# Optimization experiments

Measured on AMD Instinct MI355X. Metric: run time of the kernel, lower is better.

Reference implementation:

```python
import jax, jax.numpy as jnp
import numpy as np

EMB = 1024
HEADS = 16


def setup_inputs() -> dict:
    key = jax.random.key(0)
    ks = jax.random.split(key, 5)
    s = 1.0 / np.sqrt(EMB).astype(np.float32)
    return {
        "x": jax.random.normal(ks[0], (4, 2048, EMB), dtype=jnp.float32),
        "Wq": jax.random.normal(ks[1], (EMB, EMB), dtype=jnp.float32) * s,
        "bq": jnp.zeros((EMB,), dtype=jnp.float32),
        "Wk": jax.random.normal(ks[2], (EMB, EMB), dtype=jnp.float32) * s,
        "bk": jnp.zeros((EMB,), dtype=jnp.float32),
        "Wv": jax.random.normal(ks[3], (EMB, EMB), dtype=jnp.float32) * s,
        "bv": jnp.zeros((EMB,), dtype=jnp.float32),
        "Wo": jax.random.normal(ks[4], (EMB, EMB), dtype=jnp.float32) * s,
        "bo": jnp.zeros((EMB,), dtype=jnp.float32),
    }


def reference(x, Wq, bq, Wk, bk, Wv, bv, Wo, bo):
    b, n, e = x.shape
    h = HEADS
    d = e // h
    # QKV projections, split heads: [b, n, e] -> [b, h, n, d]
    def split_heads(t):
        return t.reshape(b, n, h, d).transpose(0, 2, 1, 3)
    q = split_heads(x @ Wq + bq)
    k = split_heads(x @ Wk + bk)
    v = split_heads(x @ Wv + bv)
    # NOTE: original scales by sqrt(emb_size), not sqrt(head_dim)
    energy = jnp.einsum('bhqd,bhkd->bhqk', q, k)
    att = jax.nn.softmax(energy / jnp.sqrt(jnp.float32(e)), axis=-1)
    # dropout is identity in eval mode
    out = jnp.einsum('bhqk,bhkd->bhqd', att, v)
    out = out.transpose(0, 2, 1, 3).reshape(b, n, e)
    return out @ Wo + bo
```

## Files before the change

### kernel.cpp

```cpp
#include <hip/hip_runtime.h>

#define EMB   1024
#define SEQ   2048
#define BATCH 4
#define HEADS 16
#define HDIM  64
#define MTOT  8192

typedef __bf16 bf16x8 __attribute__((ext_vector_type(8)));
typedef float  fx4    __attribute__((ext_vector_type(4)));

#if __has_builtin(__builtin_amdgcn_exp2f)
#define EXP2(x) __builtin_amdgcn_exp2f(x)
#else
#define EXP2(x) exp2f(x)
#endif

__device__ __forceinline__ unsigned short f2bf(float f) {
    unsigned u = __builtin_bit_cast(unsigned, f);
    u += 0x7fffu + ((u >> 16) & 1u);
    return (unsigned short)(u >> 16);
}
__device__ __forceinline__ unsigned short bfbits(float f) {
    __bf16 h = (__bf16)f;
    return __builtin_bit_cast(unsigned short, h);
}

#define AS1 __attribute__((address_space(1)))
#define AS3 __attribute__((address_space(3)))
__device__ __forceinline__ void glds16(const void* g, void* l) {
    __builtin_amdgcn_global_load_lds((AS1 void*)g, (AS3 void*)l, 16, 0, 0);
}
#define DRAIN_GLDS() __builtin_amdgcn_s_waitcnt(0x0f70)

#define BAR()    asm volatile("s_barrier" ::: "memory")
#define WAITV8() asm volatile("s_waitcnt vmcnt(8)" ::: "memory")
#define WAITV4() asm volatile("s_waitcnt vmcnt(4)" ::: "memory")
#define WAITV0() asm volatile("s_waitcnt vmcnt(0)" ::: "memory")

#define QSCALE 0.0450842137604569f

__global__ __launch_bounds__(256) void cvt_x_kernel(const float* __restrict__ x,
                                                    unsigned short* __restrict__ xb)
{
    const int idx = (blockIdx.x * 256 + threadIdx.x) * 4;
    const float4 v = *(const float4*)(x + idx);
    ushort4 o;
    o.x = f2bf(v.x); o.y = f2bf(v.y); o.z = f2bf(v.z); o.w = f2bf(v.w);
    *(ushort4*)(xb + idx) = o;
}

__global__ __launch_bounds__(256) void cvt_w_kernel(
    const float* __restrict__ w0, const float* __restrict__ w1,
    const float* __restrict__ w2, const float* __restrict__ w3,
    unsigned short* __restrict__ o0, unsigned short* __restrict__ o1,
    unsigned short* __restrict__ o2, unsigned short* __restrict__ o3)
{
    const int z = blockIdx.z;
    const float* W = z == 0 ? w0 : (z == 1 ? w1 : (z == 2 ? w2 : w3));
    unsigned short* O = z == 0 ? o0 : (z == 1 ? o1 : (z == 2 ? o2 : o3));

    __shared__ float Ws[64][65];
    const int t  = threadIdx.x;
    const int k0 = blockIdx.x * 64, n0 = blockIdx.y * 64;
#pragma unroll
    for (int p = 0; p < 4; ++p) {
        const int row = p * 16 + (t >> 4);
        const int col = (t & 15) * 4;
        const float4 v = *(const float4*)(W + (size_t)(k0 + row) * EMB + n0 + col);
        Ws[row][col]     = v.x; Ws[row][col + 1] = v.y;
        Ws[row][col + 2] = v.z; Ws[row][col + 3] = v.w;
    }
    __syncthreads();
    const int nn = t >> 2;
    const int kb = (t & 3) * 16;
#pragma unroll
    for (int q = 0; q < 2; ++q) {
        const int kk = kb + q * 8;
        ushort4 u0, u1;
        u0.x = f2bf(Ws[kk + 0][nn]); u0.y = f2bf(Ws[kk + 1][nn]);
        u0.z = f2bf(Ws[kk + 2][nn]); u0.w = f2bf(Ws[kk + 3][nn]);
        u1.x = f2bf(Ws[kk + 4][nn]); u1.y = f2bf(Ws[kk + 5][nn]);
        u1.z = f2bf(Ws[kk + 6][nn]); u1.w = f2bf(Ws[kk + 7][nn]);
        *(ushort4*)(O + (size_t)(n0 + nn) * EMB + k0 + kk)     = u0;
        *(ushort4*)(O + (size_t)(n0 + nn) * EMB + k0 + kk + 4) = u1;
    }
}

__global__ __launch_bounds__(512, 2) void gemm_qkv8p_kernel(
    const unsigned short* __restrict__ Xg, const unsigned short* __restrict__ Wg,
    const float* __restrict__ bq, const float* __restrict__ bk,
    const float* __restrict__ bv,
    unsigned short* __restrict__ qb, unsigned short* __restrict__ kb,
    unsigned short* __restrict__ vtb)
{
    __shared__ unsigned short Ls[4][2][128][64];

    int lin = blockIdx.x;
    lin = (lin & 7) * 48 + (lin >> 3);
    const int bx  = lin & 31;
    const int by  = lin >> 5;
    const int m0  = bx * 256;
    const int e0g = by * 256;

    const int t    = threadIdx.x;
    const int w    = t >> 6;
    const int lane = t & 63;
    const int low4 = lane & 15;
    const int quad = lane >> 4;
    const int wm   = w >> 2;
    const int wn   = w & 3;

    const int mat = w >> 2;
    const int wr  = w & 3;
    const int lrl = lane >> 3;
    const int cch = lane & 7;
    const int org = cch ^ lrl;
    const int grow0 = (mat ? e0g : m0) + wr * 64 + 2 * lrl + (org >> 2);
    const unsigned short* gsrc =
        (mat ? Wg : Xg) + (size_t)grow0 * EMB + (org & 3) * 8;

    const int l2  = low4 >> 1;
    const int cs8 = (((((low4 & 1) << 2) | quad)) ^ l2) * 8;

    fx4 acc[4][8] = {};

#pragma unroll
    for (int j = 0; j < 3; ++j) {
        const unsigned short* gp = gsrc + j * 32;
        glds16(gp,            &Ls[j][mat][wr * 32 +  0][0]);
        glds16(gp + 16 * EMB, &Ls[j][mat][wr * 32 +  8][0]);
        glds16(gp + 32 * EMB, &Ls[j][mat][wr * 32 + 16][0]);
        glds16(gp + 48 * EMB, &Ls[j][mat][wr * 32 + 24][0]);
    }
    WAITV8();
    BAR();

    for (int s = 0; s < 32; ++s) {
        const int slot  = s & 3;
        const int slotd = (s + 3) & 3;
        const bool st   = (s + 3 < 32);
        const unsigned short* gp = gsrc + (s + 3) * 32;
        unsigned short (*LX)[64] = Ls[slot][0];
        unsigned short (*LW)[64] = Ls[slot][1];

        bf16x8 af[4], xf[4];
#pragma unroll
        for (int ni = 0; ni < 4; ++ni)
            af[ni] = *(const bf16x8*)&LW[wn * 32 + ni * 8 + l2][cs8];
#pragma unroll
        for (int j = 0; j < 4; ++j)
            xf[j] = *(const bf16x8*)&LX[wm * 64 + j * 8 + l2][cs8];
        if (st) {
            glds16(gp,            &Ls[slotd][mat][wr * 32 + 0][0]);
            glds16(gp + 16 * EMB, &Ls[slotd][mat][wr * 32 + 8][0]);
        }
        BAR();
        __builtin_amdgcn_s_setprio(1);
#pragma unroll
        for (int ni = 0; ni < 4; ++ni)
#pragma unroll
            for (int j = 0; j < 4; ++j)
                acc[ni][j] = __builtin_amdgcn_mfma_f32_16x16x32_bf16(
                    af[ni], xf[j], acc[ni][j], 0, 0, 0);
        __builtin_amdgcn_s_setprio(0);
        BAR();

        bf16x8 xg[4];
#pragma unroll
        for (int j = 0; j < 4; ++j)
            xg[j] = *(const bf16x8*)&LX[wm * 64 + 32 + j * 8 + l2][cs8];
        if (st) {
            glds16(gp + 32 * EMB, &Ls[slotd][mat][wr * 32 + 16][0]);
            glds16(gp + 48 * EMB, &Ls[slotd][mat][wr * 32 + 24][0]);
        }
        if (s < 29)       WAITV8();
        else if (s == 29) WAITV4();
        else              WAITV0();
        BAR();
        __builtin_amdgcn_s_setprio(1);
#pragma unroll
        for (int ni = 0; ni < 4; ++ni)
#pragma unroll
            for (int j = 0; j < 4; ++j)
                acc[ni][4 + j] = __builtin_amdgcn_mfma_f32_16x16x32_bf16(
                    af[ni], xg[j], acc[ni][4 + j], 0, 0, 0);
        __builtin_amdgcn_s_setprio(0);
        BAR();
    }

    const int z   = by >> 2;
    const int eLb = (by & 3) * 256 + wn * 64;
    const float* bias = z == 0 ? bq : (z == 1 ? bk : bv);
    fx4 bvv[4];
#pragma unroll
    for (int ni = 0; ni < 4; ++ni)
        bvv[ni] = *(const fx4*)(bias + eLb + ni * 16 + quad * 4);

    if (z <= 1) {
        const float scl = (z == 0) ? QSCALE : 1.0f;
        unsigned short* o = (z == 0) ? qb : kb;
#pragma unroll
        for (int ni = 0; ni < 4; ++ni)
#pragma unroll
            for (int mi = 0; mi < 8; ++mi) {
                const int m  = m0 + wm * 128 + mi * 16 + low4;
                const int eL = eLb + ni * 16 + quad * 4;
                const int bb = m >> 11, n = m & (SEQ - 1);
                const int hh = eL >> 6, db = eL & 63;
                ushort4 o4;
                o4.x = f2bf((acc[ni][mi][0] + bvv[ni][0]) * scl);
                o4.y = f2bf((acc[ni][mi][1] + bvv[ni][1]) * scl);
                o4.z = f2bf((acc[ni][mi][2] + bvv[ni][2]) * scl);
                o4.w = f2bf((acc[ni][mi][3] + bvv[ni][3]) * scl);
                *(ushort4*)(o + (((size_t)(bb * HEADS + hh)) * SEQ + n) * HDIM + db) = o4;
            }
    } else {
        unsigned short* o = vtb;
#pragma unroll
        for (int ni = 0; ni < 4; ++ni) {
            const int eL = eLb + ni * 16 + quad * 4;
            const int hh = eL >> 6, db = eL & 63;
#pragma unroll
            for (int g = 0; g < 2; ++g) {
                const int mb = m0 + wm * 128 + g * 64;
                const int bb = mb >> 11;
                const int nb = mb & (SEQ - 1);
#pragma unroll
                for (int rr = 0; rr < 4; ++rr) {
                    ushort4 o4;
                    o4.x = f2bf(acc[ni][g * 4 + 0][rr] + bvv[ni][rr]);
                    o4.y = f2bf(acc[ni][g * 4 + 1][rr] + bvv[ni][rr]);
                    o4.z = f2bf(acc[ni][g * 4 + 2][rr] + bvv[ni][rr]);
                    o4.w = f2bf(acc[ni][g * 4 + 3][rr] + bvv[ni][rr]);
                    *(ushort4*)(o + (((size_t)(bb * HEADS + hh)) * HDIM + db + rr) * SEQ
                                  + nb + low4 * 4) = o4;
                }
            }
        }
    }
}

__global__ __launch_bounds__(256) void gemm_bf16_kernel(
    const unsigned short* __restrict__ Ag,
    const unsigned short* __restrict__ B0, const unsigned short* __restrict__ B1,
    const unsigned short* __restrict__ B2,
    const float* __restrict__ bias0, const float* __restrict__ bias1,
    const float* __restrict__ bias2,
    void* out0, void* out1, void* out2, int mode)
{
    const int z = blockIdx.z;
    const unsigned short* __restrict__ Bg = z == 0 ? B0 : (z == 1 ? B1 : B2);
    const float* __restrict__ bias = z == 0 ? bias0 : (z == 1 ? bias1 : bias2);
    void* outp = z == 0 ? out0 : (z == 1 ? out1 : out2);

    __shared__ unsigned short As[128][64];
    __shared__ unsigned short Bs[128][64];

    const int t    = threadIdx.x;
    const int w    = t >> 6;
    const int lane = t & 63;
    const int low4 = lane & 15;
    const int quad = lane >> 4;
    const int m0 = blockIdx.x * 128;
    const int e0 = blockIdx.y * 128;
    const int we = (w & 1) * 64;
    const int wm = (w >> 1) * 64;

    const int srow8  = lane >> 3;
    const int schunk = (lane & 7) ^ srow8;

    fx4 acc[4][4] = {};

    for (int k0 = 0; k0 < EMB; k0 += 64) {
        __syncthreads();
        const unsigned short* ap = Ag + (size_t)(m0 + w * 32 + srow8) * EMB + k0 + schunk * 8;
        const unsigned short* bp = Bg + (size_t)(e0 + w * 32 + srow8) * EMB + k0 + schunk * 8;
        glds16(ap,            &As[w * 32 +  0][0]);
        glds16(ap +  8 * EMB, &As[w * 32 +  8][0]);
        glds16(ap + 16 * EMB, &As[w * 32 + 16][0]);
        glds16(ap + 24 * EMB, &As[w * 32 + 24][0]);
        glds16(bp,            &Bs[w * 32 +  0][0]);
        glds16(bp +  8 * EMB, &Bs[w * 32 +  8][0]);
        glds16(bp + 16 * EMB, &Bs[w * 32 + 16][0]);
        glds16(bp + 24 * EMB, &Bs[w * 32 + 24][0]);
        DRAIN_GLDS();
        __syncthreads();

#pragma unroll
        for (int ks = 0; ks < 2; ++ks) {
            const int fch = ((ks * 4 + quad) ^ (low4 & 7)) * 8;
            bf16x8 af[4], bfr[4];
#pragma unroll
            for (int i = 0; i < 4; ++i)
                af[i] = *(const bf16x8*)&Bs[we + i * 16 + low4][fch];
#pragma unroll
            for (int j = 0; j < 4; ++j)
                bfr[j] = *(const bf16x8*)&As[wm + j * 16 + low4][fch];
#pragma unroll
            for (int i = 0; i < 4; ++i)
#pragma unroll
                for (int j = 0; j < 4; ++j)
                    acc[i][j] = __builtin_amdgcn_mfma_f32_16x16x32_bf16(af[i], bfr[j], acc[i][j], 0, 0, 0);
        }
    }

    fx4 bv[4];
#pragma unroll
    for (int i = 0; i < 4; ++i)
        bv[i] = *(const fx4*)(bias + e0 + we + i * 16 + quad * 4);

    if (mode == 1) {
#pragma unroll
        for (int i = 0; i < 4; ++i)
#pragma unroll
            for (int j = 0; j < 4; ++j) {
                const int m  = m0 + wm + j * 16 + low4;
                const int eb = e0 + we + i * 16 + quad * 4;
                fx4 o4;
#pragma unroll
                for (int rr = 0; rr < 4; ++rr) o4[rr] = acc[i][j][rr] + bv[i][rr];
                *(fx4*)((float*)outp + (size_t)m * EMB + eb) = o4;
            }
    } else if (z <= 1) {
        const float sc = (z == 0) ? QSCALE : 1.0f;
        unsigned short* o = (unsigned short*)outp;
#pragma unroll
        for (int i = 0; i < 4; ++i)
#pragma unroll
            for (int j = 0; j < 4; ++j) {
                const int m  = m0 + wm + j * 16 + low4;
                const int eb = e0 + we + i * 16 + quad * 4;
                const int bb = m >> 11, n = m & (SEQ - 1);
                const int hh = eb >> 6, db = eb & 63;
                ushort4 o4;
                o4.x = f2bf((acc[i][j][0] + bv[i][0]) * sc);
                o4.y = f2bf((acc[i][j][1] + bv[i][1]) * sc);
                o4.z = f2bf((acc[i][j][2] + bv[i][2]) * sc);
                o4.w = f2bf((acc[i][j][3] + bv[i][3]) * sc);
                *(ushort4*)(o + (((size_t)(bb * HEADS + hh)) * SEQ + n) * HDIM + db) = o4;
            }
    } else {
        unsigned short* o = (unsigned short*)outp;
        const int mbase = m0 + wm;
        const int bb    = mbase >> 11;
        const int nb    = mbase & (SEQ - 1);
#pragma unroll
        for (int i = 0; i < 4; ++i) {
            const int eb = e0 + we + i * 16 + quad * 4;
            const int hh = eb >> 6, db = eb & 63;
#pragma unroll
            for (int rr = 0; rr < 4; ++rr) {
                ushort4 o4;
                o4.x = f2bf(acc[i][0][rr] + bv[i][rr]);
                o4.y = f2bf(acc[i][1][rr] + bv[i][rr]);
                o4.z = f2bf(acc[i][2][rr] + bv[i][rr]);
                o4.w = f2bf(acc[i][3][rr] + bv[i][rr]);
                *(ushort4*)(o + (((size_t)(bb * HEADS + hh)) * HDIM + db + rr) * SEQ
                              + nb + low4 * 4) = o4;
            }
        }
    }
}

__global__ __launch_bounds__(256, 2) void attn_mfma5_kernel(
    const unsigned short* __restrict__ qg, const unsigned short* __restrict__ kg,
    const unsigned short* __restrict__ vg, unsigned short* __restrict__ attb)
{
    __shared__ unsigned short Ks[2][64][64];
    __shared__ unsigned short Vs[2][64][64];

    const int t    = threadIdx.x;
    const int w    = t >> 6;
    const int lane = t & 63;
    const int low4 = lane & 15;
    const int quad = lane >> 4;
    const int q0   = blockIdx.x * 256 + w * 64;
    const int bh   = blockIdx.y;
    const size_t base = (size_t)bh * SEQ * HDIM;

    const int srow8  = lane >> 3;
    const int schunk = (lane & 7) ^ srow8;

    const int tr  = 2 * (low4 >> 2) + (low4 & 1) + 8 * ((low4 >> 1) & 1);
    const int x7k = tr & 7;
    const int x7v = low4 & 7;

    bf16x8 aq[4][2];
#pragma unroll
    for (int s = 0; s < 4; ++s) {
        const size_t qrow = base + (size_t)(q0 + s * 16 + low4) * HDIM;
        aq[s][0] = *(const bf16x8*)(qg + qrow + quad * 8);
        aq[s][1] = *(const bf16x8*)(qg + qrow + 32 + quad * 8);
    }

    fx4 o_acc[4][4] = {};
    float l_part[4] = {};
    const fx4 fzero = {0.f, 0.f, 0.f, 0.f};

    {
        const unsigned short* kp = kg + base + (size_t)(w * 16 + srow8) * HDIM + schunk * 8;
        glds16(kp,              &Ks[0][w * 16][0]);
        glds16(kp + 8 * HDIM,   &Ks[0][w * 16 + 8][0]);
        const unsigned short* vp = vg + base + (size_t)(w * 16 + srow8) * SEQ + schunk * 8;
        glds16(vp,              &Vs[0][w * 16][0]);
        glds16(vp + 8 * SEQ,    &Vs[0][w * 16 + 8][0]);
    }

    for (int tt0 = 0; tt0 < SEQ / 64; ++tt0) {
        const int buf = tt0 & 1;
        DRAIN_GLDS();
        __syncthreads();

        bf16x8 kf[4][2], vf[4][2];
#pragma unroll
        for (int tk = 0; tk < 4; ++tk) {
#pragma unroll
            for (int c = 0; c < 2; ++c) {
                kf[tk][c] = *(const bf16x8*)&Ks[buf][tk * 16 + tr][(((c * 4 + quad) ^ x7k)) * 8];
                vf[tk][c] = *(const bf16x8*)&Vs[buf][tk * 16 + low4][(((c * 4 + quad) ^ x7v)) * 8];
            }
        }

        if (tt0 + 1 < SEQ / 64) {
            const int kv1 = (tt0 + 1) * 64;
            const unsigned short* kp = kg + base + (size_t)(kv1 + w * 16 + srow8) * HDIM + schunk * 8;
            glds16(kp,            &Ks[buf ^ 1][w * 16][0]);
            glds16(kp + 8 * HDIM, &Ks[buf ^ 1][w * 16 + 8][0]);
            const unsigned short* vp = vg + base + (size_t)(w * 16 + srow8) * SEQ + kv1 + schunk * 8;
            glds16(vp,            &Vs[buf ^ 1][w * 16][0]);
            glds16(vp + 8 * SEQ,  &Vs[buf ^ 1][w * 16 + 8][0]);
        }

#pragma unroll
        for (int s = 0; s < 4; ++s) {
            fx4 sa[4];
#pragma unroll
            for (int tk = 0; tk < 4; ++tk) {
                sa[tk] = __builtin_amdgcn_mfma_f32_16x16x32_bf16(kf[tk][0], aq[s][0], fzero, 0, 0, 0);
                sa[tk] = __builtin_amdgcn_mfma_f32_16x16x32_bf16(kf[tk][1], aq[s][1], sa[tk], 0, 0, 0);
            }
            float p[4][4];
#pragma unroll
            for (int tk = 0; tk < 4; ++tk)
#pragma unroll
                for (int r = 0; r < 4; ++r)
                    p[tk][r] = EXP2(sa[tk][r]);

            l_part[s] += (((p[0][0] + p[0][1]) + (p[0][2] + p[0][3]))
                        + ((p[1][0] + p[1][1]) + (p[1][2] + p[1][3])))
                       + (((p[2][0] + p[2][1]) + (p[2][2] + p[2][3]))
                        + ((p[3][0] + p[3][1]) + (p[3][2] + p[3][3])));

            bf16x8 pf0, pf1;
#pragma unroll
            for (int tk = 0; tk < 4; ++tk) {
                pf0[tk]     = (__bf16)p[tk][0];
                pf0[4 + tk] = (__bf16)p[tk][1];
                pf1[tk]     = (__bf16)p[tk][2];
                pf1[4 + tk] = (__bf16)p[tk][3];
            }
#pragma unroll
            for (int t2 = 0; t2 < 4; ++t2) {
                o_acc[s][t2] = __builtin_amdgcn_mfma_f32_16x16x32_bf16(vf[t2][0], pf0, o_acc[s][t2], 0, 0, 0);
                o_acc[s][t2] = __builtin_amdgcn_mfma_f32_16x16x32_bf16(vf[t2][1], pf1, o_acc[s][t2], 0, 0, 0);
            }
        }
    }

    float linv[4];
#pragma unroll
    for (int s = 0; s < 4; ++s) {
        float v = l_part[s];
        v += __shfl_xor(v, 16);
        v += __shfl_xor(v, 32);
        linv[s] = 1.0f / v;
    }

    const int bb = bh >> 4, hh = bh & 15;
#pragma unroll
    for (int s = 0; s < 4; ++s) {
        const size_t m = (size_t)bb * SEQ + q0 + s * 16 + low4;
#pragma unroll
        for (int t2 = 0; t2 < 4; ++t2) {
            ushort4 o4;
            o4.x = bfbits(o_acc[s][t2][0] * linv[s]);
            o4.y = bfbits(o_acc[s][t2][1] * linv[s]);
            o4.z = bfbits(o_acc[s][t2][2] * linv[s]);
            o4.w = bfbits(o_acc[s][t2][3] * linv[s]);
            *(ushort4*)(attb + m * EMB + hh * HDIM + t2 * 16 + quad * 4) = o4;
        }
    }
}

extern "C" void kernel_launch(void* const* d_in, const int* in_sizes, int n_in,
                              void* d_out, int out_size, void* d_ws, size_t ws_size,
                              hipStream_t stream)
{
    const float* x  = (const float*)d_in[0];
    const float* Wq = (const float*)d_in[1];
    const float* bq = (const float*)d_in[2];
    const float* Wk = (const float*)d_in[3];
    const float* bk = (const float*)d_in[4];
    const float* Wv = (const float*)d_in[5];
    const float* bv = (const float*)d_in[6];
    const float* Wo = (const float*)d_in[7];
    const float* bo = (const float*)d_in[8];

    unsigned short* ws  = (unsigned short*)d_ws;
    unsigned short* xb  = ws;
    unsigned short* wqt = xb + 8388608;
    unsigned short* wkt = wqt + 1048576;
    unsigned short* wvt = wkt + 1048576;
    unsigned short* wot = wvt + 1048576;
    unsigned short* qb  = wot + 1048576;
    unsigned short* kbuf = qb + 8388608;
    unsigned short* vtb  = kbuf + 8388608;
    unsigned short* attb = vtb + 8388608;

    cvt_x_kernel<<<8192, 256, 0, stream>>>(x, xb);
    cvt_w_kernel<<<dim3(16, 16, 4), 256, 0, stream>>>(Wq, Wk, Wv, Wo, wqt, wkt, wvt, wot);

    gemm_qkv8p_kernel<<<384, 512, 0, stream>>>(xb, wqt, bq, bk, bv, qb, kbuf, vtb);

    attn_mfma5_kernel<<<dim3(8, 64), 256, 0, stream>>>(qb, kbuf, vtb, attb);

    gemm_bf16_kernel<<<dim3(64, 8, 1), 256, 0, stream>>>(
        attb, wot, wot, wot, bo, bo, bo, d_out, d_out, d_out, 1);
}
```

Measured before the change: 275.6 us.

## Restructure QKV GEMM to double-buffered LDS with one sync per k-step

The QKV projection GEMM moves from a 4-slot LDS ring with split half-step loads and four barriers per iteration to a 2-slot double buffer. Each k-step now loads all fragments up front, waits on LDS reads, then issues the next prefetch into the same slot before running all MFMAs. This halves LDS use and raises the launch-bounds occupancy hint from 2 to 4 blocks, aiming to cut barrier overhead and raise occupancy. The trade-offs are a shallower prefetch distance, which may expose global-load latency, and more fragment registers live at once under the tighter register budget.

```diff
diff --git a/kernel.cpp b/kernel.cpp
--- a/kernel.cpp
+++ b/kernel.cpp
@@ -33,10 +33,10 @@
 }
 #define DRAIN_GLDS() __builtin_amdgcn_s_waitcnt(0x0f70)
 
-#define BAR()    asm volatile("s_barrier" ::: "memory")
-#define WAITV8() asm volatile("s_waitcnt vmcnt(8)" ::: "memory")
-#define WAITV4() asm volatile("s_waitcnt vmcnt(4)" ::: "memory")
-#define WAITV0() asm volatile("s_waitcnt vmcnt(0)" ::: "memory")
+#define BAR()     asm volatile("s_barrier" ::: "memory")
+#define WAITV4()  asm volatile("s_waitcnt vmcnt(4)" ::: "memory")
+#define WAITV0()  asm volatile("s_waitcnt vmcnt(0)" ::: "memory")
+#define WAITLG0() asm volatile("s_waitcnt lgkmcnt(0)" ::: "memory")
 
 #define QSCALE 0.0450842137604569f
 
@@ -87,14 +87,14 @@
     }
 }
 
-__global__ __launch_bounds__(512, 2) void gemm_qkv8p_kernel(
+__global__ __launch_bounds__(512, 4) void gemm_qkv2s_kernel(
     const unsigned short* __restrict__ Xg, const unsigned short* __restrict__ Wg,
     const float* __restrict__ bq, const float* __restrict__ bk,
     const float* __restrict__ bv,
     unsigned short* __restrict__ qb, unsigned short* __restrict__ kb,
     unsigned short* __restrict__ vtb)
 {
-    __shared__ unsigned short Ls[4][2][128][64];
+    __shared__ unsigned short Ls[2][2][128][64];
 
     int lin = blockIdx.x;
     lin = (lin & 7) * 48 + (lin >> 3);
@@ -123,69 +123,51 @@
     const int l2  = low4 >> 1;
     const int cs8 = (((((low4 & 1) << 2) | quad)) ^ l2) * 8;
 
+    auto stageS = [&](int slot, int sub) {
+        const unsigned short* gp = gsrc + sub * 32;
+        glds16(gp,            &Ls[slot][mat][wr * 32 +  0][0]);
+        glds16(gp + 16 * EMB, &Ls[slot][mat][wr * 32 +  8][0]);
+        glds16(gp + 32 * EMB, &Ls[slot][mat][wr * 32 + 16][0]);
+        glds16(gp + 48 * EMB, &Ls[slot][mat][wr * 32 + 24][0]);
+    };
+
     fx4 acc[4][8] = {};
 
-#pragma unroll
-    for (int j = 0; j < 3; ++j) {
-        const unsigned short* gp = gsrc + j * 32;
-        glds16(gp,            &Ls[j][mat][wr * 32 +  0][0]);
-        glds16(gp + 16 * EMB, &Ls[j][mat][wr * 32 +  8][0]);
-        glds16(gp + 32 * EMB, &Ls[j][mat][wr * 32 + 16][0]);
-        glds16(gp + 48 * EMB, &Ls[j][mat][wr * 32 + 24][0]);
-    }
-    WAITV8();
+    stageS(0, 0);
+    stageS(1, 1);
+    WAITV4();
     BAR();
 
+#pragma unroll 2
     for (int s = 0; s < 32; ++s) {
-        const int slot  = s & 3;
-        const int slotd = (s + 3) & 3;
-        const bool st   = (s + 3 < 32);
-        const unsigned short* gp = gsrc + (s + 3) * 32;
+        const int slot = s & 1;
         unsigned short (*LX)[64] = Ls[slot][0];
         unsigned short (*LW)[64] = Ls[slot][1];
 
-        bf16x8 af[4], xf[4];
+        bf16x8 af[4], xf[8];
 #pragma unroll
         for (int ni = 0; ni < 4; ++ni)
             af[ni] = *(const bf16x8*)&LW[wn * 32 + ni * 8 + l2][cs8];
 #pragma unroll
-        for (int j = 0; j < 4; ++j)
+        for (int j = 0; j < 8; ++j)
             xf[j] = *(const bf16x8*)&LX[wm * 64 + j * 8 + l2][cs8];
-        if (st) {
-            glds16(gp,            &Ls[slotd][mat][wr * 32 + 0][0]);
-            glds16(gp + 16 * EMB, &Ls[slotd][mat][wr * 32 + 8][0]);
-        }
+
+        WAITLG0();
         BAR();
+
+        if (s <= 29) stageS(slot, s + 2);
+
         __builtin_amdgcn_s_setprio(1);
 #pragma unroll
         for (int ni = 0; ni < 4; ++ni)
 #pragma unroll
-            for (int j = 0; j < 4; ++j)
+            for (int j = 0; j < 8; ++j)
                 acc[ni][j] = __builtin_amdgcn_mfma_f32_16x16x32_bf16(
                     af[ni], xf[j], acc[ni][j], 0, 0, 0);
         __builtin_amdgcn_s_setprio(0);
-        BAR();
-
-        bf16x8 xg[4];
-#pragma unroll
-        for (int j = 0; j < 4; ++j)
-            xg[j] = *(const bf16x8*)&LX[wm * 64 + 32 + j * 8 + l2][cs8];
-        if (st) {
-            glds16(gp + 32 * EMB, &Ls[slotd][mat][wr * 32 + 16][0]);
-            glds16(gp + 48 * EMB, &Ls[slotd][mat][wr * 32 + 24][0]);
-        }
-        if (s < 29)       WAITV8();
-        else if (s == 29) WAITV4();
-        else              WAITV0();
-        BAR();
-        __builtin_amdgcn_s_setprio(1);
-#pragma unroll
-        for (int ni = 0; ni < 4; ++ni)
-#pragma unroll
-            for (int j = 0; j < 4; ++j)
-                acc[ni][4 + j] = __builtin_amdgcn_mfma_f32_16x16x32_bf16(
-                    af[ni], xg[j], acc[ni][4 + j], 0, 0, 0);
-        __builtin_amdgcn_s_setprio(0);
+
+        if (s <= 29)       WAITV4();
+        else if (s == 30)  WAITV0();
         BAR();
     }
 
@@ -521,7 +503,7 @@
     cvt_x_kernel<<<8192, 256, 0, stream>>>(x, xb);
     cvt_w_kernel<<<dim3(16, 16, 4), 256, 0, stream>>>(Wq, Wk, Wv, Wo, wqt, wkt, wvt, wot);
 
-    gemm_qkv8p_kernel<<<384, 512, 0, stream>>>(xb, wqt, bq, bk, bv, qb, kbuf, vtb);
+    gemm_qkv2s_kernel<<<384, 512, 0, stream>>>(xb, wqt, bq, bk, bv, qb, kbuf, vtb);
 
     attn_mfma5_kernel<<<dim3(8, 64), 256, 0, stream>>>(qb, kbuf, vtb, attb);
 
```

Measured after the change: 747.3 us. 2.71x slower.
